# Kernel tuning notes

Hardware: AMD Instinct MI355X
Metric: run time of the kernel (lower is better)

The kernel has to match this reference:

```python
import jax, jax.numpy as jnp
import numpy as np

N = 20000   # nodes
E = 320000  # edges (before self-loops)
D = 128     # input_dim
HID = 128   # hidden_dim
HEADS = 4


def _ln(x, g, b):
    mu = x.mean(-1, keepdims=True)
    var = x.var(-1, keepdims=True)
    return (x - mu) * jax.lax.rsqrt(var + 1e-5) * g + b


def _seg_softmax(a, seg, n):
    # numerically-stable segment softmax over destination nodes
    m = jax.ops.segment_max(a, seg, num_segments=n)
    e = jnp.exp(a - m[seg])
    s = jax.ops.segment_sum(e, seg, num_segments=n)
    return e / (s[seg] + 1e-16)


def _gatv2(x, src, dst, Wl, bl, Wr, br, att, bias, heads, c, concat, n):
    # GATv2Conv: e_ij = att . leaky_relu(xl[j] + xr[i]); softmax over i's neighbors
    xl = (x @ Wl + bl).reshape(n, heads, c)
    xr = (x @ Wr + br).reshape(n, heads, c)
    e = jax.nn.leaky_relu(xl[src] + xr[dst], 0.2)        # [E, H, C]
    a = _seg_softmax(jnp.einsum('ehc,hc->eh', e, att), dst, n)
    out = jax.ops.segment_sum(xl[src] * a[:, :, None], dst, num_segments=n)
    out = out.reshape(n, heads * c) if concat else out.mean(1)
    return out + bias


def setup_inputs() -> dict:
    key = jax.random.key(0)
    ks = iter(jax.random.split(key, 64))
    def nrm(shape, s=0.05):
        return jax.random.normal(next(ks), shape, jnp.float32) * s
    d = {}
    d['x'] = jax.random.normal(next(ks), (N, D), jnp.float32)
    d['edge_index'] = jax.random.randint(next(ks), (2, E), 0, N)
    d['fn_g'] = jnp.ones(D); d['fn_b'] = jnp.zeros(D)
    d['W_in'] = nrm((D, HID)); d['b_in'] = jnp.zeros(HID)
    d['Wl1'] = nrm((HID, HEADS * HID)); d['bl1'] = jnp.zeros(HEADS * HID)
    d['Wr1'] = nrm((HID, HEADS * HID)); d['br1'] = jnp.zeros(HEADS * HID)
    d['att1'] = nrm((HEADS, HID)); d['bg1'] = jnp.zeros(HEADS * HID)
    d['Wl2'] = nrm((HEADS * HID, HID)); d['bl2'] = jnp.zeros(HID)
    d['Wr2'] = nrm((HEADS * HID, HID)); d['br2'] = jnp.zeros(HID)
    d['att2'] = nrm((1, HID)); d['bg2'] = jnp.zeros(HID)
    d['ln1_g'] = jnp.ones(HEADS * HID); d['ln1_b'] = jnp.zeros(HEADS * HID)
    d['ln2_g'] = jnp.ones(HID); d['ln2_b'] = jnp.zeros(HID)
    for p in ['rf', 'cf', 'kf']:
        d['W' + p] = nrm((HID, HID)); d['b' + p] = jnp.zeros(HID)
        d[p + '_g'] = jnp.ones(HID); d[p + '_b'] = jnp.zeros(HID)
    d['Wr1h'] = nrm((HID, HID // 2)); d['br1h'] = jnp.zeros(HID // 2)
    d['Wr2h'] = nrm((HID // 2, HID // 4)); d['br2h'] = jnp.zeros(HID // 4)
    d['Wr3h'] = nrm((HID // 4, 1)); d['br3h'] = jnp.zeros(1)
    d['Wc1h'] = nrm((HID, HID // 2)); d['bc1h'] = jnp.zeros(HID // 2)
    d['Wc2h'] = nrm((HID // 2, 2)); d['bc2h'] = jnp.zeros(2)
    d['Wk1h'] = nrm((HID, HID // 2)); d['bk1h'] = jnp.zeros(HID // 2)
    d['Wk2h'] = nrm((HID // 2, 1)); d['bk2h'] = jnp.zeros(1)
    return d


def reference(x, edge_index, fn_g, fn_b, W_in, b_in,
              Wl1, bl1, Wr1, br1, att1, bg1,
              Wl2, bl2, Wr2, br2, att2, bg2,
              ln1_g, ln1_b, ln2_g, ln2_b,
              Wrf, brf, rf_g, rf_b, Wcf, bcf, cf_g, cf_b, Wkf, bkf, kf_g, kf_b,
              Wr1h, br1h, Wr2h, br2h, Wr3h, br3h,
              Wc1h, bc1h, Wc2h, bc2h, Wk1h, bk1h, Wk2h, bk2h):
    n = x.shape[0]
    h = _ln(x, fn_g, fn_b)
    h = jax.nn.relu(h @ W_in + b_in)
    loops = jnp.arange(n)
    src = jnp.concatenate([edge_index[0], loops])
    dst = jnp.concatenate([edge_index[1], loops])
    h = _gatv2(h, src, dst, Wl1, bl1, Wr1, br1, att1, bg1, HEADS, HID, True, n)
    h = jax.nn.elu(_ln(h, ln1_g, ln1_b))
    h = _gatv2(h, src, dst, Wl2, bl2, Wr2, br2, att2, bg2, 1, HID, False, n)
    emb = jax.nn.elu(_ln(h, ln2_g, ln2_b))
    def feat(W, b, g, bb):
        return jax.nn.relu(_ln(emb @ W + b, g, bb))
    rf = feat(Wrf, brf, rf_g, rf_b)
    cf = feat(Wcf, bcf, cf_g, cf_b)
    kf = feat(Wkf, bkf, kf_g, kf_b)
    returns_pred = jnp.tanh(jax.nn.relu(jax.nn.relu(rf @ Wr1h + br1h) @ Wr2h + br2h) @ Wr3h + br3h) * 0.1
    movement_pred = jax.nn.relu(cf @ Wc1h + bc1h) @ Wc2h + bc2h
    ranking_scores = jax.nn.sigmoid(jax.nn.relu(kf @ Wk1h + bk1h) @ Wk2h + bk2h)
    return (returns_pred, movement_pred, ranking_scores, emb)
```

## Files before the change

kernel.cpp:

```cpp
#include <hip/hip_runtime.h>
#include <cmath>

#define DEV __device__ __forceinline__
#define LOG2E 1.44269504088896340736f

typedef __attribute__((ext_vector_type(8))) short short8v;
typedef __attribute__((ext_vector_type(4))) float f32x4;

DEV float lrelu(float v) { return fmaxf(v, 0.2f * v); }
DEV float elu(float v) { return v > 0.f ? v : expm1f(v); }
DEV float plo(unsigned u) { return __uint_as_float(u << 16); }
DEV float phi(unsigned u) { return __uint_as_float(u & 0xffff0000u); }
DEV unsigned short f2bf(float f) {
  unsigned u = __float_as_uint(f);
  unsigned r = (u + 0x7fffu + ((u >> 16) & 1u)) >> 16;
  return (unsigned short)r;
}
DEV unsigned packbf(float a, float b) {
  return (unsigned)f2bf(a) | ((unsigned)f2bf(b) << 16);
}
DEV void unpack8(uint4 u, float* f) {
  f[0] = plo(u.x); f[1] = phi(u.x); f[2] = plo(u.y); f[3] = phi(u.y);
  f[4] = plo(u.z); f[5] = phi(u.z); f[6] = plo(u.w); f[7] = phi(u.w);
}

__global__ void k_count(const int* __restrict__ ei, int* __restrict__ counts,
                        int E0, int ET) {
  int e = blockIdx.x * 256 + threadIdx.x;
  if (e >= ET) return;
  int dst = (e < E0) ? ei[E0 + e] : (e - E0);
  atomicAdd(&counts[dst], 1);
}

__global__ __launch_bounds__(1024) void k_scan2(const int* __restrict__ counts,
                                                int* __restrict__ offs, int n) {
  int t = threadIdx.x;
  int ch = (n + 1023) >> 10;
  int beg = t * ch, end = min(beg + ch, n);
  int loc = 0;
  for (int i = beg; i < end; ++i) loc += counts[i];
  int lane = t & 63, w = t >> 6;
  int v = loc;
#pragma unroll
  for (int m = 1; m < 64; m <<= 1) {
    int u = __shfl_up(v, m);
    if (lane >= m) v += u;
  }
  __shared__ int wsum[16], wpre[16];
  if (lane == 63) wsum[w] = v;
  __syncthreads();
  if (t < 16) {
    int p = 0;
    for (int i = 0; i < t; ++i) p += wsum[i];
    wpre[t] = p;
  }
  __syncthreads();
  int run = wpre[w] + v - loc;
  for (int i = beg; i < end; ++i) { offs[i] = run; run += counts[i]; }
  if (beg < n && end == n) offs[n] = run;
}

__global__ void k_scatter(const int* __restrict__ ei, const int* __restrict__ offs,
                          int* __restrict__ cursor, int* __restrict__ src_s,
                          int E0, int ET) {
  int e = blockIdx.x * 256 + threadIdx.x;
  if (e >= ET) return;
  int src, dst;
  if (e < E0) { src = ei[e]; dst = ei[E0 + e]; }
  else        { src = e - E0; dst = e - E0; }
  int pos = offs[dst] + atomicAdd(&cursor[dst], 1);
  src_s[pos] = src;
}

DEV void pack_one(const float* __restrict__ W, unsigned short* __restrict__ Wp,
                  int K, int N, int idx) {
  if (idx >= K * N) return;
  int j = idx & 7, l = (idx >> 3) & 63, r = idx >> 9;
  int KB = K / 32;
  int tile = r / KB, kb = r - tile * KB;
  int k = kb * 32 + (l >> 4) * 8 + j;
  int col = tile * 16 + (l & 15);
  Wp[idx] = f2bf(W[(size_t)k * N + col]);
}

__global__ void k_pack_all(const float* w0, const float* w1, const float* w2,
                           const float* w3, const float* w4, const float* w5,
                           const float* w6, const float* w7,
                           unsigned short* p0, unsigned short* p1, unsigned short* p2,
                           unsigned short* p3, unsigned short* p4, unsigned short* p5,
                           unsigned short* p6, unsigned short* p7,
                           const float* bl1, const float* br1, float* bcatA,
                           const float* bl2, const float* br2, float* bcatB) {
  int idx = blockIdx.x * 256 + threadIdx.x;
  pack_one(w0, p0, 128, 128, idx);
  pack_one(w1, p1, 128, 512, idx);
  pack_one(w2, p2, 128, 512, idx);
  pack_one(w3, p3, 512, 128, idx);
  pack_one(w4, p4, 512, 128, idx);
  pack_one(w5, p5, 128, 128, idx);
  pack_one(w6, p6, 128, 128, idx);
  pack_one(w7, p7, 128, 128, idx);
  if (idx < 512) bcatA[idx] = bl1[idx];
  else if (idx < 1024) bcatA[idx] = br1[idx - 512];
  if (idx < 128) bcatB[idx] = bl2[idx];
  else if (idx < 256) bcatB[idx] = br2[idx - 128];
}

DEV float bd1_val(const float* Wr, const float* Wc, const float* Wk, int k, int col) {
  int blk = col >> 6;
  if ((k >> 7) != blk) return 0.f;
  const float* W = (blk == 0) ? Wr : (blk == 1) ? Wc : Wk;
  return W[(k & 127) * 64 + (col & 63)];
}
DEV float bd2_val(const float* Wr2, const float* Wc2, const float* Wk2, int k, int col) {
  if (col < 32) return (k < 64) ? Wr2[k * 32 + col] : 0.f;
  if (col < 34) return (k >= 64 && k < 128) ? Wc2[(k - 64) * 2 + (col - 32)] : 0.f;
  if (col == 34) return (k >= 128) ? Wk2[k - 128] : 0.f;
  return 0.f;
}

__global__ void k_pack_heads(const float* Wr1, const float* Wc1, const float* Wk1,
                             const float* Wr2, const float* Wc2, const float* Wk2,
                             const float* br1, const float* bc1, const float* bk1,
                             const float* br2, const float* bc2, const float* bk2,
                             unsigned short* P1, unsigned short* P2,
                             float* bh1, float* bh2) {
  int idx = blockIdx.x * 256 + threadIdx.x;
  if (idx < 384 * 192) {
    int j = idx & 7, l = (idx >> 3) & 63, r = idx >> 9;
    const int KB = 12;
    int tile = r / KB, kb = r - tile * KB;
    int k = kb * 32 + (l >> 4) * 8 + j;
    int col = tile * 16 + (l & 15);
    P1[idx] = f2bf(bd1_val(Wr1, Wc1, Wk1, k, col));
  }
  if (idx < 192 * 64) {
    int j = idx & 7, l = (idx >> 3) & 63, r = idx >> 9;
    const int KB = 6;
    int tile = r / KB, kb = r - tile * KB;
    int k = kb * 32 + (l >> 4) * 8 + j;
    int col = tile * 16 + (l & 15);
    P2[idx] = f2bf(bd2_val(Wr2, Wc2, Wk2, k, col));
  }
  if (idx < 192) bh1[idx] = (idx < 64) ? br1[idx] : (idx < 128) ? bc1[idx - 64] : bk1[idx - 128];
  if (idx < 64)
    bh2[idx] = (idx < 32) ? br2[idx] : (idx < 34) ? bc2[idx - 32] : (idx == 34) ? bk2[0] : 0.f;
}

template<int K, int N, int RT, int ACT, bool OF32, bool OB16>
__global__ __launch_bounds__(256) void k_mfma(const unsigned short* __restrict__ A,
                                              const unsigned short* __restrict__ Wp,
                                              const float* __restrict__ bias,
                                              float* __restrict__ Cf,
                                              unsigned short* __restrict__ Cb) {
  constexpr int KB = K / 32;
  constexpr int TPW = N / 64;
  __shared__ short As[RT * KB * 64 * 8];
  int row0 = blockIdx.x * (16 * RT);
  int t = threadIdx.x, lane = t & 63, w = t >> 6;
  for (int idx = t; idx < RT * KB * 64; idx += 256) {
    int r = idx / (KB * 64), rem = idx - r * (KB * 64);
    int kb = rem >> 6, l = rem & 63;
    const short8v* sp = reinterpret_cast<const short8v*>(
        A + (size_t)(row0 + r * 16 + (l & 15)) * K + kb * 32 + (l >> 4) * 8);
    reinterpret_cast<short8v*>(As)[idx] = *sp;
  }
  __syncthreads();
  f32x4 acc[RT][TPW];
#pragma unroll
  for (int r = 0; r < RT; ++r)
#pragma unroll
    for (int j = 0; j < TPW; ++j) acc[r][j] = f32x4{0.f, 0.f, 0.f, 0.f};
  const short8v* Bp = reinterpret_cast<const short8v*>(Wp);
  for (int kb = 0; kb < KB; ++kb) {
    short8v a[RT];
#pragma unroll
    for (int r = 0; r < RT; ++r)
      a[r] = reinterpret_cast<const short8v*>(As)[(r * KB + kb) * 64 + lane];
#pragma unroll
    for (int j = 0; j < TPW; ++j) {
      int tile = w * TPW + j;
      short8v b = Bp[(tile * KB + kb) * 64 + lane];
#pragma unroll
      for (int r = 0; r < RT; ++r)
        acc[r][j] = __builtin_amdgcn_mfma_f32_16x16x32_bf16(a[r], b, acc[r][j], 0, 0, 0);
    }
  }
#pragma unroll
  for (int j = 0; j < TPW; ++j) {
    int col = (w * TPW + j) * 16 + (lane & 15);
    float bs = bias[col];
#pragma unroll
    for (int rt = 0; rt < RT; ++rt)
#pragma unroll
      for (int r = 0; r < 4; ++r) {
        int row = row0 + rt * 16 + (lane >> 4) * 4 + r;
        float v = acc[rt][j][r] + bs;
        if (ACT == 1) v = fmaxf(v, 0.f);
        if (OF32) Cf[(size_t)row * N + col] = v;
        if (OB16) Cb[(size_t)row * N + col] = f2bf(v);
      }
  }
}

template<int C, int ACT, bool OUT16>
__global__ void k_ln(const float* in, void* out, const float* g, const float* b) {
  constexpr int T = (C < 256) ? C : 256;
  constexpr int EPT = C / T;
  int row = blockIdx.x, t = threadIdx.x;
  const float* ip = in + (size_t)row * C;
  float v[EPT];
  float s = 0.f, s2 = 0.f;
#pragma unroll
  for (int e = 0; e < EPT; ++e) { float xv = ip[t + e * T]; v[e] = xv; s += xv; s2 += xv * xv; }
#pragma unroll
  for (int m = 1; m <= 32; m <<= 1) { s += __shfl_xor(s, m); s2 += __shfl_xor(s2, m); }
  __shared__ float w1s[2], w2s[2];
  if (T > 64) {
    if ((t & 63) == 0) { w1s[t >> 6] = s; w2s[t >> 6] = s2; }
    __syncthreads();
    s = w1s[0] + w1s[1];
    s2 = w2s[0] + w2s[1];
  }
  float mu = s * (1.0f / C);
  float var = s2 * (1.0f / C) - mu * mu;
  float rs = rsqrtf(var + 1e-5f);
#pragma unroll
  for (int e = 0; e < EPT; ++e) {
    int c = t + e * T;
    float y = (v[e] - mu) * rs * g[c] + b[c];
    if (ACT == 1) y = fmaxf(y, 0.f);
    if (ACT == 2) y = elu(y);
    if (OUT16) ((unsigned short*)out)[(size_t)row * C + c] = f2bf(y);
    else       ((float*)out)[(size_t)row * C + c] = y;
  }
}

__global__ __launch_bounds__(128) void k_gat1(const int* __restrict__ offs,
                                              const int* __restrict__ src_s,
                                              const uint4* __restrict__ xlr4,
                                              const float* __restrict__ att,
                                              const float* __restrict__ bg,
                                              const float* __restrict__ lg,
                                              const float* __restrict__ lb,
                                              uint4* __restrict__ out4,
                                              int M) {
  int w = threadIdx.x >> 6, lane = threadIdx.x & 63;
  int n = blockIdx.x * 2 + w;
  if (n >= M) return;
  int st = offs[n], en = offs[n + 1];
  int cb = lane * 8;
  uint4 ur = xlr4[(size_t)n * 128 + 64 + lane];
  float xr[8];
  unpack8(ur, xr);
  float atv[8];
  {
    const float4* atp = reinterpret_cast<const float4*>(att + cb);
    float4 a0 = atp[0], a1 = atp[1];
    atv[0] = a0.x * LOG2E; atv[1] = a0.y * LOG2E; atv[2] = a0.z * LOG2E; atv[3] = a0.w * LOG2E;
    atv[4] = a1.x * LOG2E; atv[5] = a1.y * LOG2E; atv[6] = a1.z * LOG2E; atv[7] = a1.w * LOG2E;
  }
  float m = -3.0e38f, s = 0.f;
  float acc[8];
#pragma unroll
  for (int k = 0; k < 8; ++k) acc[k] = 0.f;
  uint4 u0 = xlr4[(size_t)src_s[st] * 128 + lane];
  uint4 u1 = xlr4[(size_t)src_s[st + 1 < en ? st + 1 : st] * 128 + lane];
  for (int i = st; i < en; ++i) {
    uint4 ucur = u0;
    u0 = u1;
    int nx = (i + 2 < en) ? i + 2 : en - 1;
    u1 = xlr4[(size_t)src_s[nx] * 128 + lane];
    float xv[8];
    unpack8(ucur, xv);
    float p = 0.f;
#pragma unroll
    for (int k = 0; k < 8; ++k)
      p = fmaf(atv[k], lrelu(xv[k] + xr[k]), p);
    p += __shfl_xor(p, 1);
    p += __shfl_xor(p, 2);
    p += __shfl_xor(p, 4);
    p += __shfl_xor(p, 8);
    if (__all(p <= m)) {
      float we = exp2f(p - m);
      s += we;
#pragma unroll
      for (int k = 0; k < 8; ++k) acc[k] = fmaf(we, xv[k], acc[k]);
    } else {
      float mn = fmaxf(m, p);
      float al = exp2f(m - mn);
      float we = exp2f(p - mn);
      s = fmaf(s, al, we);
#pragma unroll
      for (int k = 0; k < 8; ++k) acc[k] = fmaf(acc[k], al, we * xv[k]);
      m = mn;
    }
  }
  float inv = 1.0f / (s + 1e-16f);
  float v[8];
  float s1 = 0.f, s2 = 0.f;
#pragma unroll
  for (int k = 0; k < 8; ++k) {
    v[k] = fmaf(acc[k], inv, bg[cb + k]);
    s1 += v[k];
    s2 += v[k] * v[k];
  }
#pragma unroll
  for (int mm = 1; mm <= 32; mm <<= 1) { s1 += __shfl_xor(s1, mm); s2 += __shfl_xor(s2, mm); }
  float mu = s1 * (1.0f / 512.0f);
  float var = s2 * (1.0f / 512.0f) - mu * mu;
  float rsd = rsqrtf(var + 1e-5f);
  float y[8];
#pragma unroll
  for (int k = 0; k < 8; ++k)
    y[k] = elu((v[k] - mu) * rsd * lg[cb + k] + lb[cb + k]);
  uint4 o;
  o.x = packbf(y[0], y[1]); o.y = packbf(y[2], y[3]);
  o.z = packbf(y[4], y[5]); o.w = packbf(y[6], y[7]);
  out4[(size_t)n * 64 + lane] = o;
}

__global__ __launch_bounds__(128) void k_gat2(const int* __restrict__ offs,
                                              const int* __restrict__ src_s,
                                              const uint4* __restrict__ xlr4,
                                              const float* __restrict__ att,
                                              const float* __restrict__ bg,
                                              const float* __restrict__ lg,
                                              const float* __restrict__ lb,
                                              float* __restrict__ emb,
                                              uint4* __restrict__ embh4,
                                              int M) {
  int w = threadIdx.x >> 6, lane = threadIdx.x & 63;
  int n = blockIdx.x * 2 + w;
  if (n >= M) return;
  int st = offs[n], en = offs[n + 1];
  int g = lane >> 4, l16 = lane & 15;
  int cb = l16 * 8;
  uint4 ur = xlr4[(size_t)n * 32 + 16 + l16];
  float xr[8];
  unpack8(ur, xr);
  float atv[8];
  {
    const float4* atp = reinterpret_cast<const float4*>(att + cb);
    float4 a0 = atp[0], a1 = atp[1];
    atv[0] = a0.x * LOG2E; atv[1] = a0.y * LOG2E; atv[2] = a0.z * LOG2E; atv[3] = a0.w * LOG2E;
    atv[4] = a1.x * LOG2E; atv[5] = a1.y * LOG2E; atv[6] = a1.z * LOG2E; atv[7] = a1.w * LOG2E;
  }
  float m = -3.0e38f, s = 0.f;
  float acc[8];
#pragma unroll
  for (int k = 0; k < 8; ++k) acc[k] = 0.f;
  int e0 = st + g, e1 = st + 4 + g;
  uint4 u0 = xlr4[(size_t)src_s[e0 < en ? e0 : en - 1] * 32 + l16];
  uint4 u1 = xlr4[(size_t)src_s[e1 < en ? e1 : en - 1] * 32 + l16];
  for (int i = st; i < en; i += 4) {
    int e = i + g;
    uint4 ucur = u0;
    u0 = u1;
    int e2 = i + 8 + g;
    u1 = xlr4[(size_t)src_s[e2 < en ? e2 : en - 1] * 32 + l16];
    float xv[8];
    unpack8(ucur, xv);
    float p = 0.f;
#pragma unroll
    for (int k = 0; k < 8; ++k)
      p = fmaf(atv[k], lrelu(xv[k] + xr[k]), p);
    p += __shfl_xor(p, 1);
    p += __shfl_xor(p, 2);
    p += __shfl_xor(p, 4);
    p += __shfl_xor(p, 8);
    if (e >= en) p = -3.0e38f;
    if (__all(p <= m)) {
      float we = exp2f(p - m);
      s += we;
#pragma unroll
      for (int k = 0; k < 8; ++k) acc[k] = fmaf(we, xv[k], acc[k]);
    } else {
      float mn = fmaxf(m, p);
      float al = exp2f(m - mn);
      float we = exp2f(p - mn);
      s = fmaf(s, al, we);
#pragma unroll
      for (int k = 0; k < 8; ++k) acc[k] = fmaf(acc[k], al, we * xv[k]);
      m = mn;
    }
  }
#pragma unroll
  for (int d = 16; d < 64; d <<= 1) {
    float mo = __shfl_xor(m, d), so = __shfl_xor(s, d);
    float ao[8];
#pragma unroll
    for (int k = 0; k < 8; ++k) ao[k] = __shfl_xor(acc[k], d);
    float mn = fmaxf(m, mo);
    float e1f = exp2f(m - mn), e2m = exp2f(mo - mn);
    s = s * e1f + so * e2m;
#pragma unroll
    for (int k = 0; k < 8; ++k) acc[k] = acc[k] * e1f + ao[k] * e2m;
    m = mn;
  }
  float inv = 1.0f / (s + 1e-16f);
  float v[8];
  float s1 = 0.f, s2 = 0.f;
#pragma unroll
  for (int k = 0; k < 8; ++k) {
    v[k] = fmaf(acc[k], inv, bg[cb + k]);
    s1 += v[k];
    s2 += v[k] * v[k];
  }
#pragma unroll
  for (int mm = 1; mm <= 32; mm <<= 1) { s1 += __shfl_xor(s1, mm); s2 += __shfl_xor(s2, mm); }
  float mu = s1 * (1.0f / 512.0f);
  float var = s2 * (1.0f / 512.0f) - mu * mu;
  float rsd = rsqrtf(var + 1e-5f);
  if (g == 0) {
    float y[8];
#pragma unroll
    for (int k = 0; k < 8; ++k)
      y[k] = elu((v[k] - mu) * rsd * lg[cb + k] + lb[cb + k]);
    float* ep = emb + (size_t)n * 128 + cb;
    *reinterpret_cast<float4*>(ep)     = float4{y[0], y[1], y[2], y[3]};
    *reinterpret_cast<float4*>(ep + 4) = float4{y[4], y[5], y[6], y[7]};
    uint4 o;
    o.x = packbf(y[0], y[1]); o.y = packbf(y[2], y[3]);
    o.z = packbf(y[4], y[5]); o.w = packbf(y[6], y[7]);
    embh4[(size_t)n * 16 + l16] = o;
  }
}

__global__ __launch_bounds__(256) void k_branch(const unsigned short* __restrict__ A,
    const unsigned short* __restrict__ Wp,
    const float* __restrict__ b0, const float* __restrict__ b1s, const float* __restrict__ b2s,
    const float* __restrict__ g0, const float* __restrict__ gb0,
    const float* __restrict__ g1, const float* __restrict__ gb1,
    const float* __restrict__ g2, const float* __restrict__ gb2,
    unsigned* __restrict__ ffh) {
  constexpr int KB = 4, TPW = 6;
  __shared__ short As[KB * 64 * 8];
  __shared__ float Cs[16 * 384];
  int row0 = blockIdx.x * 16;
  int t = threadIdx.x, lane = t & 63, w = t >> 6;
  for (int idx = t; idx < KB * 64; idx += 256) {
    int kb = idx >> 6, l = idx & 63;
    const short8v* sp = reinterpret_cast<const short8v*>(
        A + (size_t)(row0 + (l & 15)) * 128 + kb * 32 + (l >> 4) * 8);
    reinterpret_cast<short8v*>(As)[idx] = *sp;
  }
  __syncthreads();
  f32x4 acc[TPW];
#pragma unroll
  for (int j = 0; j < TPW; ++j) acc[j] = f32x4{0.f, 0.f, 0.f, 0.f};
  const short8v* Bp = reinterpret_cast<const short8v*>(Wp);
  for (int kb = 0; kb < KB; ++kb) {
    short8v a = reinterpret_cast<const short8v*>(As)[kb * 64 + lane];
#pragma unroll
    for (int j = 0; j < TPW; ++j) {
      int tile = w * TPW + j;
      short8v b = Bp[(tile * KB + kb) * 64 + lane];
      acc[j] = __builtin_amdgcn_mfma_f32_16x16x32_bf16(a, b, acc[j], 0, 0, 0);
    }
  }
#pragma unroll
  for (int j = 0; j < TPW; ++j) {
    int col = (w * TPW + j) * 16 + (lane & 15);
    int seg = col >> 7, cl = col & 127;
    const float* bp = (seg == 0) ? b0 : (seg == 1) ? b1s : b2s;
    float bs = bp[cl];
#pragma unroll
    for (int r = 0; r < 4; ++r)
      Cs[((lane >> 4) * 4 + r) * 384 + col] = acc[j][r] + bs;
  }
  __syncthreads();
  int row = t >> 4, l16 = t & 15;
#pragma unroll
  for (int seg = 0; seg < 3; ++seg) {
    float v[8];
    float s = 0.f, s2 = 0.f;
    int base = row * 384 + seg * 128 + l16 * 8;
#pragma unroll
    for (int k = 0; k < 8; ++k) { v[k] = Cs[base + k]; s += v[k]; s2 += v[k] * v[k]; }
#pragma unroll
    for (int mm = 1; mm <= 8; mm <<= 1) { s += __shfl_xor(s, mm); s2 += __shfl_xor(s2, mm); }
    float mu = s * (1.0f / 128.0f);
    float var = s2 * (1.0f / 128.0f) - mu * mu;
    float rsd = rsqrtf(var + 1e-5f);
    const float* gp = (seg == 0) ? g0 : (seg == 1) ? g1 : g2;
    const float* bp = (seg == 0) ? gb0 : (seg == 1) ? gb1 : gb2;
    unsigned* op = ffh + (size_t)(row0 + row) * 192 + seg * 64 + l16 * 4;
    float y[8];
#pragma unroll
    for (int k = 0; k < 8; ++k) {
      int c = l16 * 8 + k;
      y[k] = fmaxf((v[k] - mu) * rsd * gp[c] + bp[c], 0.f);
    }
    op[0] = packbf(y[0], y[1]); op[1] = packbf(y[2], y[3]);
    op[2] = packbf(y[4], y[5]); op[3] = packbf(y[6], y[7]);
  }
}

__global__ void k_tail(const float* __restrict__ tmp,
                       const float* __restrict__ Wr3, const float* __restrict__ br3,
                       float* __restrict__ out_ret, float* __restrict__ out_mov,
                       float* __restrict__ out_rank, int M) {
  int row = blockIdx.x * 256 + threadIdx.x;
  if (row >= M) return;
  const float4* tp = reinterpret_cast<const float4*>(tmp + (size_t)row * 64);
  float4 v[9];
#pragma unroll
  for (int q = 0; q < 9; ++q) v[q] = tp[q];
  const float* tv = reinterpret_cast<const float*>(v);
  float a3 = br3[0];
#pragma unroll
  for (int k = 0; k < 32; ++k) a3 = fmaf(fmaxf(tv[k], 0.f), Wr3[k], a3);
  out_ret[row] = tanhf(a3) * 0.1f;
  out_mov[2 * row]     = tv[32];
  out_mov[2 * row + 1] = tv[33];
  out_rank[row] = 1.0f / (1.0f + expf(-tv[34]));
}

extern "C" void kernel_launch(void* const* d_in, const int* in_sizes, int n_in,
                              void* d_out, int out_size, void* d_ws, size_t ws_size,
                              hipStream_t stream) {
  const float* x     = (const float*)d_in[0];
  const int*   ei    = (const int*)  d_in[1];
  const float* fn_g  = (const float*)d_in[2];
  const float* fn_b  = (const float*)d_in[3];
  const float* W_in  = (const float*)d_in[4];
  const float* b_in  = (const float*)d_in[5];
  const float* Wl1   = (const float*)d_in[6];
  const float* bl1   = (const float*)d_in[7];
  const float* Wr1   = (const float*)d_in[8];
  const float* br1   = (const float*)d_in[9];
  const float* att1  = (const float*)d_in[10];
  const float* bg1   = (const float*)d_in[11];
  const float* Wl2   = (const float*)d_in[12];
  const float* bl2   = (const float*)d_in[13];
  const float* Wr2   = (const float*)d_in[14];
  const float* br2   = (const float*)d_in[15];
  const float* att2  = (const float*)d_in[16];
  const float* bg2   = (const float*)d_in[17];
  const float* ln1_g = (const float*)d_in[18];
  const float* ln1_b = (const float*)d_in[19];
  const float* ln2_g = (const float*)d_in[20];
  const float* ln2_b = (const float*)d_in[21];
  const float* Wrf   = (const float*)d_in[22];
  const float* brf   = (const float*)d_in[23];
  const float* rf_g  = (const float*)d_in[24];
  const float* rf_b  = (const float*)d_in[25];
  const float* Wcf   = (const float*)d_in[26];
  const float* bcf   = (const float*)d_in[27];
  const float* cf_g  = (const float*)d_in[28];
  const float* cf_b  = (const float*)d_in[29];
  const float* Wkf   = (const float*)d_in[30];
  const float* bkf   = (const float*)d_in[31];
  const float* kf_g  = (const float*)d_in[32];
  const float* kf_b  = (const float*)d_in[33];
  const float* Wr1h  = (const float*)d_in[34];
  const float* br1h  = (const float*)d_in[35];
  const float* Wr2h  = (const float*)d_in[36];
  const float* br2h  = (const float*)d_in[37];
  const float* Wr3h  = (const float*)d_in[38];
  const float* br3h  = (const float*)d_in[39];
  const float* Wc1h  = (const float*)d_in[40];
  const float* bc1h  = (const float*)d_in[41];
  const float* Wc2h  = (const float*)d_in[42];
  const float* bc2h  = (const float*)d_in[43];
  const float* Wk1h  = (const float*)d_in[44];
  const float* bk1h  = (const float*)d_in[45];
  const float* Wk2h  = (const float*)d_in[46];
  const float* bk2h  = (const float*)d_in[47];

  const int M  = in_sizes[0] / 128;
  const int E0 = in_sizes[1] / 2;
  const int ET = E0 + M;

  char* base = (char*)d_ws;
  size_t off = 0;
  auto carve = [&](size_t bytes) -> char* {
    off = (off + 255) & ~(size_t)255;
    char* p = base + off;
    off += bytes;
    return p;
  };
  const size_t B1024 = (size_t)M * 1024 * 2;
  const size_t B512 = (size_t)M * 512 * 2;
  const size_t B256 = (size_t)M * 256 * 2;
  const size_t B128 = (size_t)M * 128 * 2;
  unsigned short* hnh   = (unsigned short*)carve(B128);
  unsigned short* h0h   = (unsigned short*)carve(B128);
  unsigned short* xlr1h = (unsigned short*)carve(B1024);
  unsigned short* g1h   = (unsigned short*)carve(B512);
  unsigned short* xlr2h = (unsigned short*)carve(B256);
  unsigned short* embh  = (unsigned short*)carve(B128);
  int* src_s = (int*)carve((size_t)(ET + 8) * sizeof(int));
  int* cnt   = (int*)carve((size_t)2 * M * sizeof(int));
  int* cur   = cnt + M;
  int* offs  = (int*)carve((size_t)(M + 1) * sizeof(int));
  unsigned short* Winp = (unsigned short*)carve(128 * 128 * 2);
  unsigned short* Wl1p = (unsigned short*)carve(128 * 512 * 2);
  unsigned short* Wr1p = (unsigned short*)carve(128 * 512 * 2);
  unsigned short* Wl2p = (unsigned short*)carve(512 * 128 * 2);
  unsigned short* Wr2p = (unsigned short*)carve(512 * 128 * 2);
  unsigned short* Wtp  = (unsigned short*)carve(3 * 128 * 128 * 2);
  unsigned short* Wh1p = (unsigned short*)carve(384 * 192 * 2);
  unsigned short* Wh2p = (unsigned short*)carve(192 * 64 * 2);
  float* bcatA = (float*)carve(1024 * sizeof(float));
  float* bcatB = (float*)carve(256 * sizeof(float));
  float* bh1  = (float*)carve(192 * sizeof(float));
  float* bh2  = (float*)carve(64 * sizeof(float));
  unsigned* ffh = (unsigned*)xlr1h;
  unsigned short* h1h = xlr1h + (size_t)M * 256;
  float* tmp = (float*)g1h;
  (void)ws_size; (void)n_in; (void)out_size; (void)Wr1p; (void)Wr2p;

  hipMemsetAsync(cnt, 0, (size_t)2 * M * sizeof(int), stream);
  k_count<<<(ET + 255) / 256, 256, 0, stream>>>(ei, cnt, E0, ET);
  k_scan2<<<1, 1024, 0, stream>>>(cnt, offs, M);
  k_scatter<<<(ET + 255) / 256, 256, 0, stream>>>(ei, offs, cur, src_s, E0, ET);

  k_pack_all<<<256, 256, 0, stream>>>(W_in, Wl1, Wr1, Wl2, Wr2, Wrf, Wcf, Wkf,
                                      Winp, Wl1p, Wr1p, Wl2p, Wr2p,
                                      Wtp, Wtp + 16384, Wtp + 32768,
                                      bl1, br1, bcatA, bl2, br2, bcatB);
  k_pack_heads<<<288, 256, 0, stream>>>(Wr1h, Wc1h, Wk1h, Wr2h, Wc2h, Wk2h,
                                        br1h, bc1h, bk1h, br2h, bc2h, bk2h,
                                        Wh1p, Wh2p, bh1, bh2);

  k_ln<128, 0, true><<<M, 128, 0, stream>>>(x, hnh, fn_g, fn_b);
  k_mfma<128, 128, 2, 1, false, true><<<M / 32, 256, 0, stream>>>(hnh, Winp, b_in, nullptr, h0h);
  k_mfma<128, 1024, 2, 0, false, true><<<M / 32, 256, 0, stream>>>(h0h, Wl1p, bcatA, nullptr, xlr1h);
  k_gat1<<<(M + 1) / 2, 128, 0, stream>>>(offs, src_s, (const uint4*)xlr1h,
                                          att1, bg1, ln1_g, ln1_b, (uint4*)g1h, M);
  k_mfma<512, 256, 2, 0, false, true><<<M / 32, 256, 0, stream>>>(g1h, Wl2p, bcatB, nullptr, xlr2h);

  float* out_ret  = (float*)d_out;
  float* out_mov  = out_ret + M;
  float* out_rank = out_ret + 3 * M;
  float* emb      = out_ret + 4 * M;
  k_gat2<<<(M + 1) / 2, 128, 0, stream>>>(offs, src_s, (const uint4*)xlr2h,
                                          att2, bg2, ln2_g, ln2_b, emb, (uint4*)embh, M);

  k_branch<<<M / 16, 256, 0, stream>>>(embh, Wtp, brf, bcf, bkf,
                                       rf_g, rf_b, cf_g, cf_b, kf_g, kf_b, ffh);

  k_mfma<384, 192, 2, 1, false, true><<<M / 32, 256, 0, stream>>>(
      (const unsigned short*)ffh, Wh1p, bh1, nullptr, h1h);
  k_mfma<192, 64, 2, 0, true, false><<<M / 32, 256, 0, stream>>>(
      h1h, Wh2p, bh2, tmp, nullptr);
  k_tail<<<(M + 255) / 256, 256, 0, stream>>>(tmp, Wr3h, br3h,
                                              out_ret, out_mov, out_rank, M);
}
```

Measured before the change: 286.4 us.

## Drop online-max softmax in GAT kernels, use packed float2 math

```diff
diff --git a/kernel.cpp b/kernel.cpp
--- a/kernel.cpp
+++ b/kernel.cpp
@@ -6,11 +6,15 @@
 
 typedef __attribute__((ext_vector_type(8))) short short8v;
 typedef __attribute__((ext_vector_type(4))) float f32x4;
+typedef __attribute__((ext_vector_type(2))) float f32x2;
 
 DEV float lrelu(float v) { return fmaxf(v, 0.2f * v); }
 DEV float elu(float v) { return v > 0.f ? v : expm1f(v); }
 DEV float plo(unsigned u) { return __uint_as_float(u << 16); }
 DEV float phi(unsigned u) { return __uint_as_float(u & 0xffff0000u); }
+DEV f32x2 pk2(unsigned u) {
+  return f32x2{__uint_as_float(u << 16), __uint_as_float(u & 0xffff0000u)};
+}
 DEV unsigned short f2bf(float f) {
   unsigned u = __float_as_uint(f);
   unsigned r = (u + 0x7fffu + ((u >> 16) & 1u)) >> 16;
@@ -18,10 +22,6 @@
 }
 DEV unsigned packbf(float a, float b) {
   return (unsigned)f2bf(a) | ((unsigned)f2bf(b) << 16);
-}
-DEV void unpack8(uint4 u, float* f) {
-  f[0] = plo(u.x); f[1] = phi(u.x); f[2] = plo(u.y); f[3] = phi(u.y);
-  f[4] = plo(u.z); f[5] = phi(u.z); f[6] = plo(u.w); f[7] = phi(u.w);
 }
 
 __global__ void k_count(const int* __restrict__ ei, int* __restrict__ counts,
@@ -236,7 +236,7 @@
   }
 }
 
-__global__ __launch_bounds__(128) void k_gat1(const int* __restrict__ offs,
+__global__ __launch_bounds__(256) void k_gat1(const int* __restrict__ offs,
                                               const int* __restrict__ src_s,
                                               const uint4* __restrict__ xlr4,
                                               const float* __restrict__ att,
@@ -246,64 +246,57 @@
                                               uint4* __restrict__ out4,
                                               int M) {
   int w = threadIdx.x >> 6, lane = threadIdx.x & 63;
-  int n = blockIdx.x * 2 + w;
+  int n = blockIdx.x * 4 + w;
   if (n >= M) return;
   int st = offs[n], en = offs[n + 1];
   int cb = lane * 8;
-  uint4 ur = xlr4[(size_t)n * 128 + 64 + lane];
-  float xr[8];
-  unpack8(ur, xr);
-  float atv[8];
+  uint4 ur = xlr4[(unsigned)n * 128u + 64u + lane];
+  f32x2 xr[4] = {pk2(ur.x), pk2(ur.y), pk2(ur.z), pk2(ur.w)};
+  f32x2 atv[4];
   {
     const float4* atp = reinterpret_cast<const float4*>(att + cb);
     float4 a0 = atp[0], a1 = atp[1];
-    atv[0] = a0.x * LOG2E; atv[1] = a0.y * LOG2E; atv[2] = a0.z * LOG2E; atv[3] = a0.w * LOG2E;
-    atv[4] = a1.x * LOG2E; atv[5] = a1.y * LOG2E; atv[6] = a1.z * LOG2E; atv[7] = a1.w * LOG2E;
-  }
-  float m = -3.0e38f, s = 0.f;
-  float acc[8];
-#pragma unroll
-  for (int k = 0; k < 8; ++k) acc[k] = 0.f;
-  uint4 u0 = xlr4[(size_t)src_s[st] * 128 + lane];
-  uint4 u1 = xlr4[(size_t)src_s[st + 1 < en ? st + 1 : st] * 128 + lane];
+    atv[0] = f32x2{a0.x, a0.y} * LOG2E;
+    atv[1] = f32x2{a0.z, a0.w} * LOG2E;
+    atv[2] = f32x2{a1.x, a1.y} * LOG2E;
+    atv[3] = f32x2{a1.z, a1.w} * LOG2E;
+  }
+  float s = 0.f;
+  f32x2 acc[4] = {f32x2{0.f, 0.f}, f32x2{0.f, 0.f}, f32x2{0.f, 0.f}, f32x2{0.f, 0.f}};
+  uint4 u0 = xlr4[(unsigned)src_s[st] * 128u + lane];
+  uint4 u1 = xlr4[(unsigned)src_s[st + 1 < en ? st + 1 : st] * 128u + lane];
   for (int i = st; i < en; ++i) {
-    uint4 ucur = u0;
+    uint4 uc = u0;
     u0 = u1;
     int nx = (i + 2 < en) ? i + 2 : en - 1;
-    u1 = xlr4[(size_t)src_s[nx] * 128 + lane];
-    float xv[8];
-    unpack8(ucur, xv);
-    float p = 0.f;
-#pragma unroll
-    for (int k = 0; k < 8; ++k)
-      p = fmaf(atv[k], lrelu(xv[k] + xr[k]), p);
+    u1 = xlr4[(unsigned)src_s[nx] * 128u + lane];
+    f32x2 xv[4] = {pk2(uc.x), pk2(uc.y), pk2(uc.z), pk2(uc.w)};
+    f32x2 ps = f32x2{0.f, 0.f};
+#pragma unroll
+    for (int k = 0; k < 4; ++k) {
+      f32x2 t = xv[k] + xr[k];
+      f32x2 lr = __builtin_elementwise_max(t, 0.2f * t);
+      ps += atv[k] * lr;
+    }
+    float p = ps.x + ps.y;
     p += __shfl_xor(p, 1);
     p += __shfl_xor(p, 2);
     p += __shfl_xor(p, 4);
     p += __shfl_xor(p, 8);
-    if (__all(p <= m)) {
-      float we = exp2f(p - m);
-      s += we;
-#pragma unroll
-      for (int k = 0; k < 8; ++k) acc[k] = fmaf(we, xv[k], acc[k]);
-    } else {
-      float mn = fmaxf(m, p);
-      float al = exp2f(m - mn);
-      float we = exp2f(p - mn);
-      s = fmaf(s, al, we);
-#pragma unroll
-      for (int k = 0; k < 8; ++k) acc[k] = fmaf(acc[k], al, we * xv[k]);
-      m = mn;
-    }
+    float we = exp2f(fminf(p, 80.f));
+    s += we;
+#pragma unroll
+    for (int k = 0; k < 4; ++k) acc[k] += we * xv[k];
   }
   float inv = 1.0f / (s + 1e-16f);
   float v[8];
   float s1 = 0.f, s2 = 0.f;
 #pragma unroll
-  for (int k = 0; k < 8; ++k) {
-    v[k] = fmaf(acc[k], inv, bg[cb + k]);
-    s1 += v[k];
-    s2 += v[k] * v[k];
+  for (int k = 0; k < 4; ++k) {
+    v[2 * k]     = fmaf(acc[k].x, inv, bg[cb + 2 * k]);
+    v[2 * k + 1] = fmaf(acc[k].y, inv, bg[cb + 2 * k + 1]);
+    s1 += v[2 * k] + v[2 * k + 1];
+    s2 += v[2 * k] * v[2 * k] + v[2 * k + 1] * v[2 * k + 1];
   }
 #pragma unroll
   for (int mm = 1; mm <= 32; mm <<= 1) { s1 += __shfl_xor(s1, mm); s2 += __shfl_xor(s2, mm); }
@@ -317,10 +310,10 @@
   uint4 o;
   o.x = packbf(y[0], y[1]); o.y = packbf(y[2], y[3]);
   o.z = packbf(y[4], y[5]); o.w = packbf(y[6], y[7]);
-  out4[(size_t)n * 64 + lane] = o;
-}
-
-__global__ __launch_bounds__(128) void k_gat2(const int* __restrict__ offs,
+  out4[(unsigned)n * 64u + lane] = o;
+}
+
+__global__ __launch_bounds__(256) void k_gat2(const int* __restrict__ offs,
                                               const int* __restrict__ src_s,
                                               const uint4* __restrict__ xlr4,
                                               const float* __restrict__ att,
@@ -331,81 +324,69 @@
                                               uint4* __restrict__ embh4,
                                               int M) {
   int w = threadIdx.x >> 6, lane = threadIdx.x & 63;
-  int n = blockIdx.x * 2 + w;
+  int n = blockIdx.x * 4 + w;
   if (n >= M) return;
   int st = offs[n], en = offs[n + 1];
   int g = lane >> 4, l16 = lane & 15;
   int cb = l16 * 8;
-  uint4 ur = xlr4[(size_t)n * 32 + 16 + l16];
-  float xr[8];
-  unpack8(ur, xr);
-  float atv[8];
+  uint4 ur = xlr4[(unsigned)n * 32u + 16u + l16];
+  f32x2 xr[4] = {pk2(ur.x), pk2(ur.y), pk2(ur.z), pk2(ur.w)};
+  f32x2 atv[4];
   {
     const float4* atp = reinterpret_cast<const float4*>(att + cb);
     float4 a0 = atp[0], a1 = atp[1];
-    atv[0] = a0.x * LOG2E; atv[1] = a0.y * LOG2E; atv[2] = a0.z * LOG2E; atv[3] = a0.w * LOG2E;
-    atv[4] = a1.x * LOG2E; atv[5] = a1.y * LOG2E; atv[6] = a1.z * LOG2E; atv[7] = a1.w * LOG2E;
-  }
-  float m = -3.0e38f, s = 0.f;
-  float acc[8];
-#pragma unroll
-  for (int k = 0; k < 8; ++k) acc[k] = 0.f;
+    atv[0] = f32x2{a0.x, a0.y} * LOG2E;
+    atv[1] = f32x2{a0.z, a0.w} * LOG2E;
+    atv[2] = f32x2{a1.x, a1.y} * LOG2E;
+    atv[3] = f32x2{a1.z, a1.w} * LOG2E;
+  }
+  float s = 0.f;
+  f32x2 acc[4] = {f32x2{0.f, 0.f}, f32x2{0.f, 0.f}, f32x2{0.f, 0.f}, f32x2{0.f, 0.f}};
   int e0 = st + g, e1 = st + 4 + g;
-  uint4 u0 = xlr4[(size_t)src_s[e0 < en ? e0 : en - 1] * 32 + l16];
-  uint4 u1 = xlr4[(size_t)src_s[e1 < en ? e1 : en - 1] * 32 + l16];
+  uint4 u0 = xlr4[(unsigned)src_s[e0 < en ? e0 : en - 1] * 32u + l16];
+  uint4 u1 = xlr4[(unsigned)src_s[e1 < en ? e1 : en - 1] * 32u + l16];
   for (int i = st; i < en; i += 4) {
     int e = i + g;
-    uint4 ucur = u0;
+    uint4 uc = u0;
     u0 = u1;
     int e2 = i + 8 + g;
-    u1 = xlr4[(size_t)src_s[e2 < en ? e2 : en - 1] * 32 + l16];
-    float xv[8];
-    unpack8(ucur, xv);
-    float p = 0.f;
-#pragma unroll
-    for (int k = 0; k < 8; ++k)
-      p = fmaf(atv[k], lrelu(xv[k] + xr[k]), p);
+    u1 = xlr4[(unsigned)src_s[e2 < en ? e2 : en - 1] * 32u + l16];
+    f32x2 xv[4] = {pk2(uc.x), pk2(uc.y), pk2(uc.z), pk2(uc.w)};
+    f32x2 ps = f32x2{0.f, 0.f};
+#pragma unroll
+    for (int k = 0; k < 4; ++k) {
+      f32x2 t = xv[k] + xr[k];
+      f32x2 lr = __builtin_elementwise_max(t, 0.2f * t);
+      ps += atv[k] * lr;
+    }
+    float p = ps.x + ps.y;
     p += __shfl_xor(p, 1);
     p += __shfl_xor(p, 2);
     p += __shfl_xor(p, 4);
     p += __shfl_xor(p, 8);
-    if (e >= en) p = -3.0e38f;
-    if (__all(p <= m)) {
-      float we = exp2f(p - m);
-      s += we;
-#pragma unroll
-      for (int k = 0; k < 8; ++k) acc[k] = fmaf(we, xv[k], acc[k]);
-    } else {
-      float mn = fmaxf(m, p);
-      float al = exp2f(m - mn);
-      float we = exp2f(p - mn);
-      s = fmaf(s, al, we);
-#pragma unroll
-      for (int k = 0; k < 8; ++k) acc[k] = fmaf(acc[k], al, we * xv[k]);
-      m = mn;
+    float we = (e < en) ? exp2f(fminf(p, 80.f)) : 0.f;
+    s += we;
+#pragma unroll
+    for (int k = 0; k < 4; ++k) acc[k] += we * xv[k];
+  }
+#pragma unroll
+  for (int d = 16; d < 64; d <<= 1) {
+    s += __shfl_xor(s, d);
+#pragma unroll
+    for (int k = 0; k < 4; ++k) {
+      acc[k].x += __shfl_xor(acc[k].x, d);
+      acc[k].y += __shfl_xor(acc[k].y, d);
     }
-  }
-#pragma unroll
-  for (int d = 16; d < 64; d <<= 1) {
-    float mo = __shfl_xor(m, d), so = __shfl_xor(s, d);
-    float ao[8];
-#pragma unroll
-    for (int k = 0; k < 8; ++k) ao[k] = __shfl_xor(acc[k], d);
-    float mn = fmaxf(m, mo);
-    float e1f = exp2f(m - mn), e2m = exp2f(mo - mn);
-    s = s * e1f + so * e2m;
-#pragma unroll
-    for (int k = 0; k < 8; ++k) acc[k] = acc[k] * e1f + ao[k] * e2m;
-    m = mn;
   }
   float inv = 1.0f / (s + 1e-16f);
   float v[8];
   float s1 = 0.f, s2 = 0.f;
 #pragma unroll
-  for (int k = 0; k < 8; ++k) {
-    v[k] = fmaf(acc[k], inv, bg[cb + k]);
-    s1 += v[k];
-    s2 += v[k] * v[k];
+  for (int k = 0; k < 4; ++k) {
+    v[2 * k]     = fmaf(acc[k].x, inv, bg[cb + 2 * k]);
+    v[2 * k + 1] = fmaf(acc[k].y, inv, bg[cb + 2 * k + 1]);
+    s1 += v[2 * k] + v[2 * k + 1];
+    s2 += v[2 * k] * v[2 * k] + v[2 * k + 1] * v[2 * k + 1];
   }
 #pragma unroll
   for (int mm = 1; mm <= 32; mm <<= 1) { s1 += __shfl_xor(s1, mm); s2 += __shfl_xor(s2, mm); }
@@ -423,7 +404,7 @@
     uint4 o;
     o.x = packbf(y[0], y[1]); o.y = packbf(y[2], y[3]);
     o.z = packbf(y[4], y[5]); o.w = packbf(y[6], y[7]);
-    embh4[(size_t)n * 16 + l16] = o;
+    embh4[(unsigned)n * 16u + l16] = o;
   }
 }
 
@@ -628,7 +609,7 @@
   k_ln<128, 0, true><<<M, 128, 0, stream>>>(x, hnh, fn_g, fn_b);
   k_mfma<128, 128, 2, 1, false, true><<<M / 32, 256, 0, stream>>>(hnh, Winp, b_in, nullptr, h0h);
   k_mfma<128, 1024, 2, 0, false, true><<<M / 32, 256, 0, stream>>>(h0h, Wl1p, bcatA, nullptr, xlr1h);
-  k_gat1<<<(M + 1) / 2, 128, 0, stream>>>(offs, src_s, (const uint4*)xlr1h,
+  k_gat1<<<(M + 3) / 4, 256, 0, stream>>>(offs, src_s, (const uint4*)xlr1h,
                                           att1, bg1, ln1_g, ln1_b, (uint4*)g1h, M);
   k_mfma<512, 256, 2, 0, false, true><<<M / 32, 256, 0, stream>>>(g1h, Wl2p, bcatB, nullptr, xlr2h);
 
@@ -636,7 +617,7 @@
   float* out_mov  = out_ret + M;
   float* out_rank = out_ret + 3 * M;
   float* emb      = out_ret + 4 * M;
-  k_gat2<<<(M + 1) / 2, 128, 0, stream>>>(offs, src_s, (const uint4*)xlr2h,
+  k_gat2<<<(M + 3) / 4, 256, 0, stream>>>(offs, src_s, (const uint4*)xlr2h,
                                           att2, bg2, ln2_g, ln2_b, emb, (uint4*)embh, M);
 
   k_branch<<<M / 16, 256, 0, stream>>>(embh, Wtp, brf, bcf, bkf,
```

Measured after the change: 288.5 us. Within noise of the previous version (+0.7%).
